# Kernel optimization log

Measured on AMD Instinct MI355X. Metric: run time of the kernel, lower is better.

The kernel has to match this reference:

```python
import jax, jax.numpy as jnp
import numpy as np

N_NODES = 50000
N_EDGES = 800000
D = 128
L = 3


def setup_inputs() -> dict:
    key = jax.random.key(0)
    ks = jax.random.split(key, 16)
    x = jax.random.normal(ks[0], (N_NODES, D), dtype=jnp.float32)
    edge_index = jax.random.randint(ks[1], (2, N_EDGES), 0, N_NODES, dtype=jnp.int32)
    # ensure every node has at least one incoming edge (degree > 0)
    edge_index = edge_index.at[1, :N_NODES].set(jnp.arange(N_NODES, dtype=jnp.int32))
    edge_attr = jax.random.normal(ks[2], (N_EDGES, 1), dtype=jnp.float32)
    s = 1.0 / np.sqrt(D)
    lin_w = jax.random.normal(ks[3], (L, 1, D), dtype=jnp.float32)          # edge_dim=1 -> D
    lin_b = jax.random.normal(ks[4], (L, D), dtype=jnp.float32) * s
    eps = jnp.zeros((L,), dtype=jnp.float32)                                 # initial_eps = 0, trainable
    w1 = jax.random.normal(ks[5], (L, D, D), dtype=jnp.float32) * s
    b1 = jax.random.normal(ks[6], (L, D), dtype=jnp.float32) * s
    w2 = jax.random.normal(ks[7], (L, D, D), dtype=jnp.float32) * s
    b2 = jax.random.normal(ks[8], (L, D), dtype=jnp.float32) * s
    d_cat = D + L * D
    final_w = jax.random.normal(ks[9], (d_cat, D), dtype=jnp.float32) / np.sqrt(d_cat)
    final_b = jax.random.normal(ks[10], (D,), dtype=jnp.float32) * s
    return {"x": x, "edge_index": edge_index, "edge_attr": edge_attr,
            "lin_w": lin_w, "lin_b": lin_b, "eps": eps,
            "w1": w1, "b1": b1, "w2": w2, "b2": b2,
            "final_w": final_w, "final_b": final_b}


def reference(x, edge_index, edge_attr, lin_w, lin_b, eps, w1, b1, w2, b2, final_w, final_b):
    src, tgt = edge_index[0], edge_index[1]
    n = x.shape[0]
    # degree of target nodes (float), shape [N, 1]
    deg = jax.ops.segment_sum(jnp.ones(src.shape[0], x.dtype), tgt, num_segments=n)[:, None]
    xs = [x]
    h = x
    for l in range(L):
        e = edge_attr @ lin_w[l] + lin_b[l]                  # [E, D] edge-feature projection
        msg = jax.nn.relu(h[src] + e)                        # gather + fuse + relu
        agg = jax.ops.segment_sum(msg, tgt, num_segments=n)  # scatter-add
        out = agg / deg + (1.0 + eps[l]) * h                 # degree-normalize + eps-residual
        h = jax.nn.relu(out @ w1[l] + b1[l]) @ w2[l] + b2[l] # 2-layer MLP (no BN, no dropout)
        xs.append(h)
    cat = jnp.concatenate(xs, axis=-1)                       # [N, D + L*D]
    return cat @ final_w + final_b
```

## Files before the change

kernel.cpp:

```cpp
#include <hip/hip_runtime.h>

#define NN 50000
#define NE 800000
#define DIM 128
#define NLAYERS 3

typedef __attribute__((ext_vector_type(8))) short bf16x8;
typedef __attribute__((ext_vector_type(4))) float f32x4;

__device__ __forceinline__ unsigned short f2bf_hi(float f) {
    unsigned int u = __float_as_uint(f);
    u += 0x7FFF + ((u >> 16) & 1);
    return (unsigned short)(u >> 16);
}
__device__ __forceinline__ float bf2f(unsigned short u) {
    return __uint_as_float(((unsigned int)u) << 16);
}

__global__ __launch_bounds__(256) void rank_kernel(const int* __restrict__ tgt,
                                                   int* __restrict__ counts,
                                                   int* __restrict__ rank, int E) {
    int base = (blockIdx.x * 256 + threadIdx.x) * 4;
    if (base >= E) return;
    int4 t = *(const int4*)(tgt + base);
    int4 r;
    r.x = atomicAdd(&counts[t.x], 1);
    r.y = atomicAdd(&counts[t.y], 1);
    r.z = atomicAdd(&counts[t.z], 1);
    r.w = atomicAdd(&counts[t.w], 1);
    *(int4*)(rank + base) = r;
}

__global__ __launch_bounds__(256) void scan_partial_kernel(const int* __restrict__ counts,
                                                           int* __restrict__ psum, int n) {
    __shared__ int ws[4];
    int b = blockIdx.x, t = threadIdx.x;
    int idx = b * 1024 + t * 4;
    int v = 0;
    if (idx < n) {
        int4 c = *(const int4*)(counts + idx);
        v = c.x + c.y + c.z + c.w;
    }
#pragma unroll
    for (int o = 32; o > 0; o >>= 1) v += __shfl_xor(v, o);
    int lane = t & 63, wid = t >> 6;
    if (lane == 0) ws[wid] = v;
    __syncthreads();
    if (t == 0) psum[b] = ws[0] + ws[1] + ws[2] + ws[3];
}

__global__ __launch_bounds__(64) void scan_small_kernel(const int* __restrict__ psum,
                                                        int* __restrict__ pbase,
                                                        int* __restrict__ offsets,
                                                        int nb, int n) {
    int lane = threadIdx.x;
    int v = (lane < nb) ? psum[lane] : 0;
    int incl = v;
#pragma unroll
    for (int o = 1; o < 64; o <<= 1) {
        int t = __shfl_up(incl, o);
        if (lane >= o) incl += t;
    }
    if (lane < nb) pbase[lane] = incl - v;
    if (lane == 63) offsets[n] = incl;
}

__global__ __launch_bounds__(256) void scan_apply_kernel(const int* __restrict__ counts,
                                                         const int* __restrict__ pbase,
                                                         int* __restrict__ offsets, int n) {
    __shared__ int ws[4];
    int b = blockIdx.x, t = threadIdx.x;
    int lane = t & 63, wid = t >> 6;
    int idx = b * 1024 + t * 4;
    int4 c = make_int4(0, 0, 0, 0);
    if (idx < n) c = *(const int4*)(counts + idx);
    int tsum = c.x + c.y + c.z + c.w;
    int incl = tsum;
#pragma unroll
    for (int o = 1; o < 64; o <<= 1) {
        int tt = __shfl_up(incl, o);
        if (lane >= o) incl += tt;
    }
    if (lane == 63) ws[wid] = incl;
    __syncthreads();
    int wbase = pbase[b];
    for (int w = 0; w < wid; w++) wbase += ws[w];
    if (idx < n) {
        int e0 = wbase + incl - tsum;
        int4 o;
        o.x = e0;
        o.y = e0 + c.x;
        o.z = o.y + c.y;
        o.w = o.z + c.z;
        *(int4*)(offsets + idx) = o;
    }
}

__global__ __launch_bounds__(256) void scatter2_kernel(
    const int* __restrict__ src, const int* __restrict__ tgt,
    const float* __restrict__ ea, const int* __restrict__ rank,
    const int* __restrict__ offsets, int2* __restrict__ sedge, int E) {
    int base = (blockIdx.x * 256 + threadIdx.x) * 4;
    if (base >= E) return;
    int4 s = *(const int4*)(src + base);
    int4 t = *(const int4*)(tgt + base);
    int4 r = *(const int4*)(rank + base);
    float4 a = *(const float4*)(ea + base);
    sedge[offsets[t.x] + r.x] = make_int2(s.x << 8, __float_as_int(a.x));
    sedge[offsets[t.y] + r.y] = make_int2(s.y << 8, __float_as_int(a.y));
    sedge[offsets[t.z] + r.z] = make_int2(s.z << 8, __float_as_int(a.z));
    sedge[offsets[t.w] + r.w] = make_int2(s.w << 8, __float_as_int(a.w));
}

__global__ __launch_bounds__(256) void xcvt_kernel(const float* __restrict__ x,
                                                   unsigned short* __restrict__ xb, int n) {
    int i = (blockIdx.x * 256 + threadIdx.x) * 4;
    if (i >= n) return;
    float4 v = *(const float4*)(x + i);
    ushort4 o;
    o.x = f2bf_hi(v.x); o.y = f2bf_hi(v.y);
    o.z = f2bf_hi(v.z); o.w = f2bf_hi(v.w);
    *(ushort4*)(xb + i) = o;
}

__global__ __launch_bounds__(256) void agg_kernel(
    const unsigned short* __restrict__ hprev, const int* __restrict__ offs,
    const int2* __restrict__ sedge,
    const float* __restrict__ lw, const float* __restrict__ lb,
    const float* __restrict__ epsp, int layer,
    float* __restrict__ outb, int N) {
    int wv = threadIdx.x >> 6;
    int node = blockIdx.x * 4 + wv;
    if (node >= N) return;
    int lane = threadIdx.x & 63;
    int q = lane >> 4, r = lane & 15;
    int d0 = r * 8;
    float lwv[8], lbv[8];
    *(float4*)&lwv[0] = *(const float4*)(lw + d0);
    *(float4*)&lwv[4] = *(const float4*)(lw + d0 + 4);
    *(float4*)&lbv[0] = *(const float4*)(lb + d0);
    *(float4*)&lbv[4] = *(const float4*)(lb + d0 + 4);
    int s0 = offs[node], s1 = offs[node + 1];
    int cnt = s1 - s0;
    float a[8];
#pragma unroll
    for (int c = 0; c < 8; c++) a[c] = 0.f;

    const char* hbase = (const char*)hprev + r * 16;

    int idx = s0 + q;
    int2 e0 = sedge[min(idx, s1 - 1)];
    int2 e1 = sedge[min(idx + 4, s1 - 1)];
    int2 e2 = sedge[min(idx + 8, s1 - 1)];
    uint4 h0 = *(const uint4*)(hbase + (unsigned)e0.x);
    uint4 h1 = *(const uint4*)(hbase + (unsigned)e1.x);

    for (int it = idx; it < s1; it += 4) {
        uint4 h2 = *(const uint4*)(hbase + (unsigned)e2.x);
        int2 e3 = sedge[min(it + 12, s1 - 1)];
        float wgt = __int_as_float(e0.y);
        unsigned uu[4] = {h0.x, h0.y, h0.z, h0.w};
#pragma unroll
        for (int c = 0; c < 4; c++) {
            float f0 = __uint_as_float(uu[c] << 16);
            float f1 = __uint_as_float(uu[c] & 0xffff0000u);
            a[2 * c]     += fmaxf(f0 + fmaf(wgt, lwv[2 * c], lbv[2 * c]), 0.f);
            a[2 * c + 1] += fmaxf(f1 + fmaf(wgt, lwv[2 * c + 1], lbv[2 * c + 1]), 0.f);
        }
        e0 = e1; e1 = e2; e2 = e3;
        h0 = h1; h1 = h2;
    }

#pragma unroll
    for (int c = 0; c < 8; c++) {
        a[c] += __shfl_xor(a[c], 16);
        a[c] += __shfl_xor(a[c], 32);
    }

    if (q == 0) {
        float inv = 1.f / (float)cnt;
        float ge = 1.f + epsp[layer];
        uint4 hs = *(const uint4*)(hbase + ((unsigned)node << 8));
        unsigned su[4] = {hs.x, hs.y, hs.z, hs.w};
        float o[8];
#pragma unroll
        for (int c = 0; c < 4; c++) {
            float f0 = __uint_as_float(su[c] << 16);
            float f1 = __uint_as_float(su[c] & 0xffff0000u);
            o[2 * c]     = a[2 * c] * inv + ge * f0;
            o[2 * c + 1] = a[2 * c + 1] * inv + ge * f1;
        }
        float* op = outb + (size_t)node * DIM + d0;
        *(float4*)op = *(float4*)&o[0];
        *(float4*)(op + 4) = *(float4*)&o[4];
    }
}

__global__ __launch_bounds__(256) void wprep_kernel(
    const float* __restrict__ w1, const float* __restrict__ w2, const float* __restrict__ fw,
    unsigned short* __restrict__ w1t_h, unsigned short* __restrict__ w1t_l,
    unsigned short* __restrict__ w2t_h, unsigned short* __restrict__ w2t_l,
    unsigned short* __restrict__ fwt_h, unsigned short* __restrict__ fwt_l) {
    int gid = blockIdx.x * 256 + threadIdx.x;
    float v; int oidx;
    unsigned short *oh, *ol;
    if (gid < 49152) {
        int l = gid >> 14, rem = gid & 16383, k = rem >> 7, c = rem & 127;
        v = w1[gid]; oidx = l * 16384 + c * 128 + k; oh = w1t_h; ol = w1t_l;
    } else if (gid < 98304) {
        int g = gid - 49152;
        int l = g >> 14, rem = g & 16383, k = rem >> 7, c = rem & 127;
        v = w2[g]; oidx = l * 16384 + c * 128 + k; oh = w2t_h; ol = w2t_l;
    } else if (gid < 163840) {
        int g = gid - 98304;
        int k = g >> 7, c = g & 127;
        v = fw[g]; oidx = c * 512 + k; oh = fwt_h; ol = fwt_l;
    } else return;
    unsigned short h = f2bf_hi(v);
    float lo = v - bf2f(h);
    oh[oidx] = h;
    ol[oidx] = f2bf_hi(lo);
}

#define AST 40
#define WST 40

__global__ __launch_bounds__(256) void mlp_fused(
    const float* __restrict__ in,
    const unsigned short* __restrict__ w1h, const unsigned short* __restrict__ w1l,
    const float* __restrict__ b1,
    const unsigned short* __restrict__ w2h, const unsigned short* __restrict__ w2l,
    const float* __restrict__ b2,
    unsigned short* __restrict__ out, int N) {
    __shared__ float s_h[64][132];
    __shared__ unsigned short s_ah[64 * AST], s_al[64 * AST];
    __shared__ unsigned short s_wh[128 * WST], s_wl[128 * WST];
    int tid = threadIdx.x;
    int n0 = blockIdx.x * 64;
    int lane = tid & 63, w = tid >> 6;
    int q = lane >> 4, lr = lane & 15;
    int wr = w >> 1, wc = w & 1;
    int sar = tid >> 2, sak = (tid & 3) * 8;
    int swc = tid >> 1, sws = (tid & 1) * 16;

    f32x4 acc[2][4];
#pragma unroll
    for (int i = 0; i < 2; i++)
#pragma unroll
        for (int j = 0; j < 4; j++) acc[i][j] = (f32x4)(0.f);

    for (int k0 = 0; k0 < 128; k0 += 32) {
        float f[8] = {0.f, 0.f, 0.f, 0.f, 0.f, 0.f, 0.f, 0.f};
        if (n0 + sar < NN) {
            const float* ap = in + (size_t)(n0 + sar) * 128 + k0 + sak;
            float4 v0 = *(const float4*)ap;
            float4 v1 = *(const float4*)(ap + 4);
            f[0] = v0.x; f[1] = v0.y; f[2] = v0.z; f[3] = v0.w;
            f[4] = v1.x; f[5] = v1.y; f[6] = v1.z; f[7] = v1.w;
        }
        unsigned int uh[4], ul[4];
#pragma unroll
        for (int i = 0; i < 4; i++) {
            unsigned short h0 = f2bf_hi(f[2 * i]);
            unsigned short h1 = f2bf_hi(f[2 * i + 1]);
            unsigned short l0 = f2bf_hi(f[2 * i] - bf2f(h0));
            unsigned short l1 = f2bf_hi(f[2 * i + 1] - bf2f(h1));
            uh[i] = (unsigned int)h0 | ((unsigned int)h1 << 16);
            ul[i] = (unsigned int)l0 | ((unsigned int)l1 << 16);
        }
        *(uint4*)&s_ah[sar * AST + sak] = make_uint4(uh[0], uh[1], uh[2], uh[3]);
        *(uint4*)&s_al[sar * AST + sak] = make_uint4(ul[0], ul[1], ul[2], ul[3]);
        {
            const unsigned short* wph = w1h + (size_t)swc * 128 + k0 + sws;
            const unsigned short* wpl = w1l + (size_t)swc * 128 + k0 + sws;
            uint4 h0 = *(const uint4*)wph;
            uint4 h1 = *(const uint4*)(wph + 8);
            uint4 l0 = *(const uint4*)wpl;
            uint4 l1 = *(const uint4*)(wpl + 8);
            *(uint4*)&s_wh[swc * WST + sws] = h0;
            *(uint4*)&s_wh[swc * WST + sws + 8] = h1;
            *(uint4*)&s_wl[swc * WST + sws] = l0;
            *(uint4*)&s_wl[swc * WST + sws + 8] = l1;
        }
        __syncthreads();
        bf16x8 ah[2], al_[2], bh[4], bl[4];
#pragma unroll
        for (int i = 0; i < 2; i++) {
            int row = wr * 32 + i * 16 + lr;
            ah[i]  = *(const bf16x8*)&s_ah[row * AST + q * 8];
            al_[i] = *(const bf16x8*)&s_al[row * AST + q * 8];
        }
#pragma unroll
        for (int j = 0; j < 4; j++) {
            int col = wc * 64 + j * 16 + lr;
            bh[j] = *(const bf16x8*)&s_wh[col * WST + q * 8];
            bl[j] = *(const bf16x8*)&s_wl[col * WST + q * 8];
        }
#pragma unroll
        for (int i = 0; i < 2; i++)
#pragma unroll
            for (int j = 0; j < 4; j++) {
                acc[i][j] = __builtin_amdgcn_mfma_f32_16x16x32_bf16(ah[i], bh[j], acc[i][j], 0, 0, 0);
                acc[i][j] = __builtin_amdgcn_mfma_f32_16x16x32_bf16(ah[i], bl[j], acc[i][j], 0, 0, 0);
                acc[i][j] = __builtin_amdgcn_mfma_f32_16x16x32_bf16(al_[i], bh[j], acc[i][j], 0, 0, 0);
            }
        __syncthreads();
    }
#pragma unroll
    for (int i = 0; i < 2; i++) {
        int rbase = wr * 32 + i * 16 + q * 4;
#pragma unroll
        for (int j = 0; j < 4; j++) {
            int col = wc * 64 + j * 16 + lr;
            float bv = b1[col];
#pragma unroll
            for (int r = 0; r < 4; r++)
                s_h[rbase + r][col] = fmaxf(acc[i][j][r] + bv, 0.f);
        }
    }
    __syncthreads();

#pragma unroll
    for (int i = 0; i < 2; i++)
#pragma unroll
        for (int j = 0; j < 4; j++) acc[i][j] = (f32x4)(0.f);

    for (int k0 = 0; k0 < 128; k0 += 32) {
        float f[8];
        *(float4*)&f[0] = *(const float4*)&s_h[sar][k0 + sak];
        *(float4*)&f[4] = *(const float4*)&s_h[sar][k0 + sak + 4];
        unsigned int uh[4], ul[4];
#pragma unroll
        for (int i = 0; i < 4; i++) {
            unsigned short h0 = f2bf_hi(f[2 * i]);
            unsigned short h1 = f2bf_hi(f[2 * i + 1]);
            unsigned short l0 = f2bf_hi(f[2 * i] - bf2f(h0));
            unsigned short l1 = f2bf_hi(f[2 * i + 1] - bf2f(h1));
            uh[i] = (unsigned int)h0 | ((unsigned int)h1 << 16);
            ul[i] = (unsigned int)l0 | ((unsigned int)l1 << 16);
        }
        __syncthreads();
        *(uint4*)&s_ah[sar * AST + sak] = make_uint4(uh[0], uh[1], uh[2], uh[3]);
        *(uint4*)&s_al[sar * AST + sak] = make_uint4(ul[0], ul[1], ul[2], ul[3]);
        {
            const unsigned short* wph = w2h + (size_t)swc * 128 + k0 + sws;
            const unsigned short* wpl = w2l + (size_t)swc * 128 + k0 + sws;
            uint4 h0 = *(const uint4*)wph;
            uint4 h1 = *(const uint4*)(wph + 8);
            uint4 l0 = *(const uint4*)wpl;
            uint4 l1 = *(const uint4*)(wpl + 8);
            *(uint4*)&s_wh[swc * WST + sws] = h0;
            *(uint4*)&s_wh[swc * WST + sws + 8] = h1;
            *(uint4*)&s_wl[swc * WST + sws] = l0;
            *(uint4*)&s_wl[swc * WST + sws + 8] = l1;
        }
        __syncthreads();
        bf16x8 ah[2], al_[2], bh[4], bl[4];
#pragma unroll
        for (int i = 0; i < 2; i++) {
            int row = wr * 32 + i * 16 + lr;
            ah[i]  = *(const bf16x8*)&s_ah[row * AST + q * 8];
            al_[i] = *(const bf16x8*)&s_al[row * AST + q * 8];
        }
#pragma unroll
        for (int j = 0; j < 4; j++) {
            int col = wc * 64 + j * 16 + lr;
            bh[j] = *(const bf16x8*)&s_wh[col * WST + q * 8];
            bl[j] = *(const bf16x8*)&s_wl[col * WST + q * 8];
        }
#pragma unroll
        for (int i = 0; i < 2; i++)
#pragma unroll
            for (int j = 0; j < 4; j++) {
                acc[i][j] = __builtin_amdgcn_mfma_f32_16x16x32_bf16(ah[i], bh[j], acc[i][j], 0, 0, 0);
                acc[i][j] = __builtin_amdgcn_mfma_f32_16x16x32_bf16(ah[i], bl[j], acc[i][j], 0, 0, 0);
                acc[i][j] = __builtin_amdgcn_mfma_f32_16x16x32_bf16(al_[i], bh[j], acc[i][j], 0, 0, 0);
            }
    }

#pragma unroll
    for (int i = 0; i < 2; i++) {
        int rbase = wr * 32 + i * 16 + q * 4;
#pragma unroll
        for (int j = 0; j < 4; j++) {
            int col = wc * 64 + j * 16 + lr;
            float bv = b2[col];
#pragma unroll
            for (int r = 0; r < 4; r++) {
                int node = n0 + rbase + r;
                if (node < NN)
                    out[(size_t)node * 128 + col] = f2bf_hi(acc[i][j][r] + bv);
            }
        }
    }
}

__global__ __launch_bounds__(256) void final_mfma(
    const unsigned short* __restrict__ a0, const unsigned short* __restrict__ a1,
    const unsigned short* __restrict__ a2, const unsigned short* __restrict__ a3,
    const unsigned short* __restrict__ wt_h, const unsigned short* __restrict__ wt_l,
    const float* __restrict__ bias, float* __restrict__ out, int N) {
    __shared__ unsigned short s_ah[64 * AST];
    __shared__ unsigned short s_wh[128 * WST], s_wl[128 * WST];
    const unsigned short* srcs[4] = {a0, a1, a2, a3};
    const int K = 512;
    int tid = threadIdx.x;
    int n0 = blockIdx.x * 64;
    int lane = tid & 63, w = tid >> 6;
    int q = lane >> 4, lr = lane & 15;
    int wr = w >> 1, wc = w & 1;

    f32x4 acc[2][4];
#pragma unroll
    for (int i = 0; i < 2; i++)
#pragma unroll
        for (int j = 0; j < 4; j++) acc[i][j] = (f32x4)(0.f);

    int sar = tid >> 2;
    int sak = (tid & 3) * 8;
    int swc = tid >> 1;
    int sws = (tid & 1) * 16;

    for (int k0 = 0; k0 < K; k0 += 32) {
        const unsigned short* asrc = srcs[k0 >> 7];
        int kl = k0 & 127;
        uint4 av = make_uint4(0, 0, 0, 0);
        if (n0 + sar < N)
            av = *(const uint4*)(asrc + (size_t)(n0 + sar) * 128 + kl + sak);
        *(uint4*)&s_ah[sar * AST + sak] = av;
        {
            const unsigned short* wph = wt_h + (size_t)swc * K + k0 + sws;
            const unsigned short* wpl = wt_l + (size_t)swc * K + k0 + sws;
            uint4 h0 = *(const uint4*)wph;
            uint4 h1 = *(const uint4*)(wph + 8);
            uint4 l0 = *(const uint4*)wpl;
            uint4 l1 = *(const uint4*)(wpl + 8);
            *(uint4*)&s_wh[swc * WST + sws] = h0;
            *(uint4*)&s_wh[swc * WST + sws + 8] = h1;
            *(uint4*)&s_wl[swc * WST + sws] = l0;
            *(uint4*)&s_wl[swc * WST + sws + 8] = l1;
        }
        __syncthreads();
        bf16x8 ah[2], bh[4], bl[4];
#pragma unroll
        for (int i = 0; i < 2; i++) {
            int row = wr * 32 + i * 16 + lr;
            ah[i] = *(const bf16x8*)&s_ah[row * AST + q * 8];
        }
#pragma unroll
        for (int j = 0; j < 4; j++) {
            int col = wc * 64 + j * 16 + lr;
            bh[j] = *(const bf16x8*)&s_wh[col * WST + q * 8];
            bl[j] = *(const bf16x8*)&s_wl[col * WST + q * 8];
        }
#pragma unroll
        for (int i = 0; i < 2; i++)
#pragma unroll
            for (int j = 0; j < 4; j++) {
                acc[i][j] = __builtin_amdgcn_mfma_f32_16x16x32_bf16(ah[i], bh[j], acc[i][j], 0, 0, 0);
                acc[i][j] = __builtin_amdgcn_mfma_f32_16x16x32_bf16(ah[i], bl[j], acc[i][j], 0, 0, 0);
            }
        __syncthreads();
    }

#pragma unroll
    for (int i = 0; i < 2; i++) {
        int rbase = wr * 32 + i * 16 + q * 4;
#pragma unroll
        for (int j = 0; j < 4; j++) {
            int col = wc * 64 + j * 16 + lr;
            float bv = bias[col];
#pragma unroll
            for (int r = 0; r < 4; r++) {
                int node = n0 + rbase + r;
                if (node < N)
                    out[(size_t)node * 128 + col] = acc[i][j][r] + bv;
            }
        }
    }
}

extern "C" void kernel_launch(void* const* d_in, const int* in_sizes, int n_in,
                              void* d_out, int out_size, void* d_ws, size_t ws_size,
                              hipStream_t stream) {
    const float* x   = (const float*)d_in[0];
    const int* edge_index = (const int*)d_in[1];
    const float* ea  = (const float*)d_in[2];
    const float* lw  = (const float*)d_in[3];
    const float* lb  = (const float*)d_in[4];
    const float* eps = (const float*)d_in[5];
    const float* w1  = (const float*)d_in[6];
    const float* b1  = (const float*)d_in[7];
    const float* w2  = (const float*)d_in[8];
    const float* b2  = (const float*)d_in[9];
    const float* fw  = (const float*)d_in[10];
    const float* fb  = (const float*)d_in[11];
    float* out = (float*)d_out;

    const int N = NN, E = NE;
    const int* src = edge_index;
    const int* tgt = edge_index + E;
    const int NB = (N + 1023) / 1024;

    char* ws = (char*)d_ws;
    size_t off = 0;
    auto alloc = [&](size_t bytes) {
        void* p = ws + off;
        off += (bytes + 255) & ~(size_t)255;
        return p;
    };
    int*   counts  = (int*)alloc((size_t)N * 4);
    int*   offsets = (int*)alloc((size_t)(N + 1) * 4);
    int*   rank    = (int*)alloc((size_t)E * 4);
    int*   psum    = (int*)alloc((size_t)NB * 4);
    int*   pbase   = (int*)alloc((size_t)NB * 4);
    int2*  sedge   = (int2*)alloc((size_t)E * 8);
    unsigned short* w1t_h = (unsigned short*)alloc(49152 * 2);
    unsigned short* w1t_l = (unsigned short*)alloc(49152 * 2);
    unsigned short* w2t_h = (unsigned short*)alloc(49152 * 2);
    unsigned short* w2t_l = (unsigned short*)alloc(49152 * 2);
    unsigned short* fwt_h = (unsigned short*)alloc(65536 * 2);
    unsigned short* fwt_l = (unsigned short*)alloc(65536 * 2);
    unsigned short* xb    = (unsigned short*)alloc((size_t)N * DIM * 2);
    unsigned short* hbuf[3];
    for (int i = 0; i < 3; i++) hbuf[i] = (unsigned short*)alloc((size_t)N * DIM * 2);
    float* outb = (float*)alloc((size_t)N * DIM * 4);
    (void)ws_size; (void)in_sizes; (void)n_in; (void)out_size;

    hipMemsetAsync(counts, 0, (size_t)N * 4, stream);
    rank_kernel<<<(E / 4 + 255) / 256, 256, 0, stream>>>(tgt, counts, rank, E);
    wprep_kernel<<<640, 256, 0, stream>>>(w1, w2, fw, w1t_h, w1t_l, w2t_h, w2t_l, fwt_h, fwt_l);
    xcvt_kernel<<<(N * DIM / 4 + 255) / 256, 256, 0, stream>>>(x, xb, N * DIM);
    scan_partial_kernel<<<NB, 256, 0, stream>>>(counts, psum, N);
    scan_small_kernel<<<1, 64, 0, stream>>>(psum, pbase, offsets, NB, N);
    scan_apply_kernel<<<NB, 256, 0, stream>>>(counts, pbase, offsets, N);
    scatter2_kernel<<<(E / 4 + 255) / 256, 256, 0, stream>>>(src, tgt, ea, rank, offsets, sedge, E);

    const int GB = (N + 63) / 64;
    for (int l = 0; l < NLAYERS; l++) {
        const unsigned short* hin = (l == 0) ? xb : hbuf[l - 1];
        agg_kernel<<<(N + 3) / 4, 256, 0, stream>>>(hin, offsets, sedge,
            lw + l * DIM, lb + l * DIM, eps, l, outb, N);
        mlp_fused<<<GB, 256, 0, stream>>>(
            outb,
            w1t_h + l * 16384, w1t_l + l * 16384, b1 + l * DIM,
            w2t_h + l * 16384, w2t_l + l * 16384, b2 + l * DIM,
            hbuf[l], N);
    }
    final_mfma<<<GB, 256, 0, stream>>>(
        xb, hbuf[0], hbuf[1], hbuf[2], fwt_h, fwt_l, fb, out, N);
}
```

Measured before the change: 378.5 us.

## Pre-split aggregation output to bf16 hi/lo and load MFMA weights directly from packed layout

The aggregation kernel now writes bf16 hi/lo pairs instead of fp32, so the MLP no longer splits its input in registers. Weights are pre-packed into MFMA fragment order, so each wave loads its A fragments straight from global memory rather than staging them through shared memory with barriers. The MLP and final GEMM use a transposed tiling (weights as A, nodes as B) and store hidden activations to LDS as bf16 hi/lo. The trade is more global weight loads per wave, relying on cache hits, in exchange for fewer LDS round trips and syncs.

New measurement: 371.4 us. About the same (-1.9%).

```diff
diff --git a/kernel.cpp b/kernel.cpp
--- a/kernel.cpp
+++ b/kernel.cpp
@@ -128,7 +128,7 @@
     const int2* __restrict__ sedge,
     const float* __restrict__ lw, const float* __restrict__ lb,
     const float* __restrict__ epsp, int layer,
-    float* __restrict__ outb, int N) {
+    unsigned short* __restrict__ aggh, unsigned short* __restrict__ aggl, int N) {
     int wv = threadIdx.x >> 6;
     int node = blockIdx.x * 4 + wv;
     if (node >= N) return;
@@ -182,18 +182,29 @@
         float ge = 1.f + epsp[layer];
         uint4 hs = *(const uint4*)(hbase + ((unsigned)node << 8));
         unsigned su[4] = {hs.x, hs.y, hs.z, hs.w};
-        float o[8];
+        unsigned short hh[8], hl[8];
 #pragma unroll
         for (int c = 0; c < 4; c++) {
             float f0 = __uint_as_float(su[c] << 16);
             float f1 = __uint_as_float(su[c] & 0xffff0000u);
-            o[2 * c]     = a[2 * c] * inv + ge * f0;
-            o[2 * c + 1] = a[2 * c + 1] * inv + ge * f1;
-        }
-        float* op = outb + (size_t)node * DIM + d0;
-        *(float4*)op = *(float4*)&o[0];
-        *(float4*)(op + 4) = *(float4*)&o[4];
-    }
+            float v0 = a[2 * c] * inv + ge * f0;
+            float v1 = a[2 * c + 1] * inv + ge * f1;
+            unsigned short h0v = f2bf_hi(v0), h1v = f2bf_hi(v1);
+            hh[2 * c] = h0v; hh[2 * c + 1] = h1v;
+            hl[2 * c] = f2bf_hi(v0 - bf2f(h0v));
+            hl[2 * c + 1] = f2bf_hi(v1 - bf2f(h1v));
+        }
+        unsigned short* ph = aggh + (size_t)node * DIM + d0;
+        unsigned short* pl = aggl + (size_t)node * DIM + d0;
+        *(ushort4*)ph       = *(const ushort4*)&hh[0];
+        *(ushort4*)(ph + 4) = *(const ushort4*)&hh[4];
+        *(ushort4*)pl       = *(const ushort4*)&hl[0];
+        *(ushort4*)(pl + 4) = *(const ushort4*)&hl[4];
+    }
+}
+
+__device__ __forceinline__ int packidx(int k, int c) {
+    return (((k >> 5) << 3) + (c >> 4)) * 512 + (((k >> 3) & 3) << 7) + ((c & 15) << 3) + (k & 7);
 }
 
 __global__ __launch_bounds__(256) void wprep_kernel(
@@ -206,15 +217,15 @@
     unsigned short *oh, *ol;
     if (gid < 49152) {
         int l = gid >> 14, rem = gid & 16383, k = rem >> 7, c = rem & 127;
-        v = w1[gid]; oidx = l * 16384 + c * 128 + k; oh = w1t_h; ol = w1t_l;
+        v = w1[gid]; oidx = l * 16384 + packidx(k, c); oh = w1t_h; ol = w1t_l;
     } else if (gid < 98304) {
         int g = gid - 49152;
         int l = g >> 14, rem = g & 16383, k = rem >> 7, c = rem & 127;
-        v = w2[g]; oidx = l * 16384 + c * 128 + k; oh = w2t_h; ol = w2t_l;
+        v = w2[g]; oidx = l * 16384 + packidx(k, c); oh = w2t_h; ol = w2t_l;
     } else if (gid < 163840) {
         int g = gid - 98304;
         int k = g >> 7, c = g & 127;
-        v = fw[g]; oidx = c * 512 + k; oh = fwt_h; ol = fwt_l;
+        v = fw[g]; oidx = packidx(k, c); oh = fwt_h; ol = fwt_l;
     } else return;
     unsigned short h = f2bf_hi(v);
     float lo = v - bf2f(h);
@@ -222,259 +233,179 @@
     ol[oidx] = f2bf_hi(lo);
 }
 
-#define AST 40
-#define WST 40
-
-__global__ __launch_bounds__(256) void mlp_fused(
-    const float* __restrict__ in,
+#define HSTR 136
+
+__global__ __launch_bounds__(256, 4) void mlp_fused(
+    const unsigned short* __restrict__ ah_g, const unsigned short* __restrict__ al_g,
     const unsigned short* __restrict__ w1h, const unsigned short* __restrict__ w1l,
     const float* __restrict__ b1,
     const unsigned short* __restrict__ w2h, const unsigned short* __restrict__ w2l,
     const float* __restrict__ b2,
     unsigned short* __restrict__ out, int N) {
-    __shared__ float s_h[64][132];
-    __shared__ unsigned short s_ah[64 * AST], s_al[64 * AST];
-    __shared__ unsigned short s_wh[128 * WST], s_wl[128 * WST];
+    __shared__ unsigned short s_hh[64 * HSTR], s_hl[64 * HSTR];
     int tid = threadIdx.x;
-    int n0 = blockIdx.x * 64;
     int lane = tid & 63, w = tid >> 6;
     int q = lane >> 4, lr = lane & 15;
     int wr = w >> 1, wc = w & 1;
-    int sar = tid >> 2, sak = (tid & 3) * 8;
-    int swc = tid >> 1, sws = (tid & 1) * 16;
-
-    f32x4 acc[2][4];
-#pragma unroll
-    for (int i = 0; i < 2; i++)
-#pragma unroll
-        for (int j = 0; j < 4; j++) acc[i][j] = (f32x4)(0.f);
-
+    int n0 = blockIdx.x * 64;
+    int nb0 = n0 + wc * 32 + lr;
+
+    f32x4 acc[4][2];
+#pragma unroll
+    for (int i = 0; i < 4; i++)
+#pragma unroll
+        for (int j = 0; j < 2; j++) acc[i][j] = (f32x4)(0.f);
+
+#pragma unroll
     for (int k0 = 0; k0 < 128; k0 += 32) {
-        float f[8] = {0.f, 0.f, 0.f, 0.f, 0.f, 0.f, 0.f, 0.f};
-        if (n0 + sar < NN) {
-            const float* ap = in + (size_t)(n0 + sar) * 128 + k0 + sak;
-            float4 v0 = *(const float4*)ap;
-            float4 v1 = *(const float4*)(ap + 4);
-            f[0] = v0.x; f[1] = v0.y; f[2] = v0.z; f[3] = v0.w;
-            f[4] = v1.x; f[5] = v1.y; f[6] = v1.z; f[7] = v1.w;
-        }
-        unsigned int uh[4], ul[4];
+        bf16x8 Bh[2], Bl[2];
+#pragma unroll
+        for (int j = 0; j < 2; j++) {
+            size_t ro = (size_t)min(nb0 + j * 16, N - 1) * DIM + k0 + q * 8;
+            Bh[j] = *(const bf16x8*)(ah_g + ro);
+            Bl[j] = *(const bf16x8*)(al_g + ro);
+        }
 #pragma unroll
         for (int i = 0; i < 4; i++) {
-            unsigned short h0 = f2bf_hi(f[2 * i]);
-            unsigned short h1 = f2bf_hi(f[2 * i + 1]);
-            unsigned short l0 = f2bf_hi(f[2 * i] - bf2f(h0));
-            unsigned short l1 = f2bf_hi(f[2 * i + 1] - bf2f(h1));
-            uh[i] = (unsigned int)h0 | ((unsigned int)h1 << 16);
-            ul[i] = (unsigned int)l0 | ((unsigned int)l1 << 16);
-        }
-        *(uint4*)&s_ah[sar * AST + sak] = make_uint4(uh[0], uh[1], uh[2], uh[3]);
-        *(uint4*)&s_al[sar * AST + sak] = make_uint4(ul[0], ul[1], ul[2], ul[3]);
-        {
-            const unsigned short* wph = w1h + (size_t)swc * 128 + k0 + sws;
-            const unsigned short* wpl = w1l + (size_t)swc * 128 + k0 + sws;
-            uint4 h0 = *(const uint4*)wph;
-            uint4 h1 = *(const uint4*)(wph + 8);
-            uint4 l0 = *(const uint4*)wpl;
-            uint4 l1 = *(const uint4*)(wpl + 8);
-            *(uint4*)&s_wh[swc * WST + sws] = h0;
-            *(uint4*)&s_wh[swc * WST + sws + 8] = h1;
-            *(uint4*)&s_wl[swc * WST + sws] = l0;
-            *(uint4*)&s_wl[swc * WST + sws + 8] = l1;
-        }
-        __syncthreads();
-        bf16x8 ah[2], al_[2], bh[4], bl[4];
-#pragma unroll
-        for (int i = 0; i < 2; i++) {
-            int row = wr * 32 + i * 16 + lr;
-            ah[i]  = *(const bf16x8*)&s_ah[row * AST + q * 8];
-            al_[i] = *(const bf16x8*)&s_al[row * AST + q * 8];
-        }
-#pragma unroll
-        for (int j = 0; j < 4; j++) {
-            int col = wc * 64 + j * 16 + lr;
-            bh[j] = *(const bf16x8*)&s_wh[col * WST + q * 8];
-            bl[j] = *(const bf16x8*)&s_wl[col * WST + q * 8];
-        }
-#pragma unroll
-        for (int i = 0; i < 2; i++)
-#pragma unroll
-            for (int j = 0; j < 4; j++) {
-                acc[i][j] = __builtin_amdgcn_mfma_f32_16x16x32_bf16(ah[i], bh[j], acc[i][j], 0, 0, 0);
-                acc[i][j] = __builtin_amdgcn_mfma_f32_16x16x32_bf16(ah[i], bl[j], acc[i][j], 0, 0, 0);
-                acc[i][j] = __builtin_amdgcn_mfma_f32_16x16x32_bf16(al_[i], bh[j], acc[i][j], 0, 0, 0);
-            }
-        __syncthreads();
-    }
-#pragma unroll
-    for (int i = 0; i < 2; i++) {
-        int rbase = wr * 32 + i * 16 + q * 4;
-#pragma unroll
-        for (int j = 0; j < 4; j++) {
-            int col = wc * 64 + j * 16 + lr;
-            float bv = b1[col];
-#pragma unroll
-            for (int r = 0; r < 4; r++)
-                s_h[rbase + r][col] = fmaxf(acc[i][j][r] + bv, 0.f);
+            size_t co = ((size_t)((k0 >> 5) * 8 + wr * 4 + i) << 9) + lane * 8;
+            bf16x8 Ah = *(const bf16x8*)(w1h + co);
+            bf16x8 Al = *(const bf16x8*)(w1l + co);
+#pragma unroll
+            for (int j = 0; j < 2; j++) {
+                acc[i][j] = __builtin_amdgcn_mfma_f32_16x16x32_bf16(Ah, Bh[j], acc[i][j], 0, 0, 0);
+                acc[i][j] = __builtin_amdgcn_mfma_f32_16x16x32_bf16(Ah, Bl[j], acc[i][j], 0, 0, 0);
+                acc[i][j] = __builtin_amdgcn_mfma_f32_16x16x32_bf16(Al, Bh[j], acc[i][j], 0, 0, 0);
+            }
+        }
+    }
+
+#pragma unroll
+    for (int i = 0; i < 4; i++) {
+        int hc0 = wr * 64 + i * 16 + q * 4;
+        float4 bv = *(const float4*)(b1 + hc0);
+        float bvr[4] = {bv.x, bv.y, bv.z, bv.w};
+#pragma unroll
+        for (int j = 0; j < 2; j++) {
+            int nl = wc * 32 + j * 16 + lr;
+            unsigned short hh[4], hl[4];
+#pragma unroll
+            for (int r = 0; r < 4; r++) {
+                float v = fmaxf(acc[i][j][r] + bvr[r], 0.f);
+                unsigned short h = f2bf_hi(v);
+                hh[r] = h;
+                hl[r] = f2bf_hi(v - bf2f(h));
+            }
+            *(ushort4*)&s_hh[nl * HSTR + hc0] = *(const ushort4*)&hh[0];
+            *(ushort4*)&s_hl[nl * HSTR + hc0] = *(const ushort4*)&hl[0];
         }
     }
     __syncthreads();
 
 #pragma unroll
-    for (int i = 0; i < 2; i++)
-#pragma unroll
-        for (int j = 0; j < 4; j++) acc[i][j] = (f32x4)(0.f);
-
+    for (int i = 0; i < 4; i++)
+#pragma unroll
+        for (int j = 0; j < 2; j++) acc[i][j] = (f32x4)(0.f);
+
+#pragma unroll
     for (int k0 = 0; k0 < 128; k0 += 32) {
-        float f[8];
-        *(float4*)&f[0] = *(const float4*)&s_h[sar][k0 + sak];
-        *(float4*)&f[4] = *(const float4*)&s_h[sar][k0 + sak + 4];
-        unsigned int uh[4], ul[4];
+        bf16x8 Bh[2], Bl[2];
+#pragma unroll
+        for (int j = 0; j < 2; j++) {
+            int so = (wc * 32 + j * 16 + lr) * HSTR + k0 + q * 8;
+            Bh[j] = *(const bf16x8*)&s_hh[so];
+            Bl[j] = *(const bf16x8*)&s_hl[so];
+        }
 #pragma unroll
         for (int i = 0; i < 4; i++) {
-            unsigned short h0 = f2bf_hi(f[2 * i]);
-            unsigned short h1 = f2bf_hi(f[2 * i + 1]);
-            unsigned short l0 = f2bf_hi(f[2 * i] - bf2f(h0));
-            unsigned short l1 = f2bf_hi(f[2 * i + 1] - bf2f(h1));
-            uh[i] = (unsigned int)h0 | ((unsigned int)h1 << 16);
-            ul[i] = (unsigned int)l0 | ((unsigned int)l1 << 16);
-        }
-        __syncthreads();
-        *(uint4*)&s_ah[sar * AST + sak] = make_uint4(uh[0], uh[1], uh[2], uh[3]);
-        *(uint4*)&s_al[sar * AST + sak] = make_uint4(ul[0], ul[1], ul[2], ul[3]);
-        {
-            const unsigned short* wph = w2h + (size_t)swc * 128 + k0 + sws;
-            const unsigned short* wpl = w2l + (size_t)swc * 128 + k0 + sws;
-            uint4 h0 = *(const uint4*)wph;
-            uint4 h1 = *(const uint4*)(wph + 8);
-            uint4 l0 = *(const uint4*)wpl;
-            uint4 l1 = *(const uint4*)(wpl + 8);
-            *(uint4*)&s_wh[swc * WST + sws] = h0;
-            *(uint4*)&s_wh[swc * WST + sws + 8] = h1;
-            *(uint4*)&s_wl[swc * WST + sws] = l0;
-            *(uint4*)&s_wl[swc * WST + sws + 8] = l1;
-        }
-        __syncthreads();
-        bf16x8 ah[2], al_[2], bh[4], bl[4];
-#pragma unroll
-        for (int i = 0; i < 2; i++) {
-            int row = wr * 32 + i * 16 + lr;
-            ah[i]  = *(const bf16x8*)&s_ah[row * AST + q * 8];
-            al_[i] = *(const bf16x8*)&s_al[row * AST + q * 8];
-        }
-#pragma unroll
-        for (int j = 0; j < 4; j++) {
-            int col = wc * 64 + j * 16 + lr;
-            bh[j] = *(const bf16x8*)&s_wh[col * WST + q * 8];
-            bl[j] = *(const bf16x8*)&s_wl[col * WST + q * 8];
-        }
-#pragma unroll
-        for (int i = 0; i < 2; i++)
-#pragma unroll
-            for (int j = 0; j < 4; j++) {
-                acc[i][j] = __builtin_amdgcn_mfma_f32_16x16x32_bf16(ah[i], bh[j], acc[i][j], 0, 0, 0);
-                acc[i][j] = __builtin_amdgcn_mfma_f32_16x16x32_bf16(ah[i], bl[j], acc[i][j], 0, 0, 0);
-                acc[i][j] = __builtin_amdgcn_mfma_f32_16x16x32_bf16(al_[i], bh[j], acc[i][j], 0, 0, 0);
-            }
-    }
-
-#pragma unroll
-    for (int i = 0; i < 2; i++) {
-        int rbase = wr * 32 + i * 16 + q * 4;
-#pragma unroll
-        for (int j = 0; j < 4; j++) {
-            int col = wc * 64 + j * 16 + lr;
-            float bv = b2[col];
-#pragma unroll
-            for (int r = 0; r < 4; r++) {
-                int node = n0 + rbase + r;
-                if (node < NN)
-                    out[(size_t)node * 128 + col] = f2bf_hi(acc[i][j][r] + bv);
-            }
-        }
-    }
-}
-
-__global__ __launch_bounds__(256) void final_mfma(
+            size_t co = ((size_t)((k0 >> 5) * 8 + wr * 4 + i) << 9) + lane * 8;
+            bf16x8 Ah = *(const bf16x8*)(w2h + co);
+            bf16x8 Al = *(const bf16x8*)(w2l + co);
+#pragma unroll
+            for (int j = 0; j < 2; j++) {
+                acc[i][j] = __builtin_amdgcn_mfma_f32_16x16x32_bf16(Ah, Bh[j], acc[i][j], 0, 0, 0);
+                acc[i][j] = __builtin_amdgcn_mfma_f32_16x16x32_bf16(Ah, Bl[j], acc[i][j], 0, 0, 0);
+                acc[i][j] = __builtin_amdgcn_mfma_f32_16x16x32_bf16(Al, Bh[j], acc[i][j], 0, 0, 0);
+            }
+        }
+    }
+
+#pragma unroll
+    for (int i = 0; i < 4; i++) {
+        int hc0 = wr * 64 + i * 16 + q * 4;
+        float4 bv = *(const float4*)(b2 + hc0);
+        float bvr[4] = {bv.x, bv.y, bv.z, bv.w};
+#pragma unroll
+        for (int j = 0; j < 2; j++) {
+            int node = nb0 + j * 16;
+            if (node < N) {
+                unsigned short o[4];
+#pragma unroll
+                for (int r = 0; r < 4; r++) o[r] = f2bf_hi(acc[i][j][r] + bvr[r]);
+                *(ushort4*)&out[(size_t)node * DIM + hc0] = *(const ushort4*)&o[0];
+            }
+        }
+    }
+}
+
+__global__ __launch_bounds__(256, 4) void final_mfma(
     const unsigned short* __restrict__ a0, const unsigned short* __restrict__ a1,
     const unsigned short* __restrict__ a2, const unsigned short* __restrict__ a3,
-    const unsigned short* __restrict__ wt_h, const unsigned short* __restrict__ wt_l,
+    const unsigned short* __restrict__ wh, const unsigned short* __restrict__ wl,
     const float* __restrict__ bias, float* __restrict__ out, int N) {
-    __shared__ unsigned short s_ah[64 * AST];
-    __shared__ unsigned short s_wh[128 * WST], s_wl[128 * WST];
-    const unsigned short* srcs[4] = {a0, a1, a2, a3};
-    const int K = 512;
     int tid = threadIdx.x;
-    int n0 = blockIdx.x * 64;
     int lane = tid & 63, w = tid >> 6;
     int q = lane >> 4, lr = lane & 15;
     int wr = w >> 1, wc = w & 1;
-
-    f32x4 acc[2][4];
-#pragma unroll
-    for (int i = 0; i < 2; i++)
-#pragma unroll
-        for (int j = 0; j < 4; j++) acc[i][j] = (f32x4)(0.f);
-
-    int sar = tid >> 2;
-    int sak = (tid & 3) * 8;
-    int swc = tid >> 1;
-    int sws = (tid & 1) * 16;
-
-    for (int k0 = 0; k0 < K; k0 += 32) {
-        const unsigned short* asrc = srcs[k0 >> 7];
-        int kl = k0 & 127;
-        uint4 av = make_uint4(0, 0, 0, 0);
-        if (n0 + sar < N)
-            av = *(const uint4*)(asrc + (size_t)(n0 + sar) * 128 + kl + sak);
-        *(uint4*)&s_ah[sar * AST + sak] = av;
-        {
-            const unsigned short* wph = wt_h + (size_t)swc * K + k0 + sws;
-            const unsigned short* wpl = wt_l + (size_t)swc * K + k0 + sws;
-            uint4 h0 = *(const uint4*)wph;
-            uint4 h1 = *(const uint4*)(wph + 8);
-            uint4 l0 = *(const uint4*)wpl;
-            uint4 l1 = *(const uint4*)(wpl + 8);
-            *(uint4*)&s_wh[swc * WST + sws] = h0;
-            *(uint4*)&s_wh[swc * WST + sws + 8] = h1;
-            *(uint4*)&s_wl[swc * WST + sws] = l0;
-            *(uint4*)&s_wl[swc * WST + sws + 8] = l1;
-        }
-        __syncthreads();
-        bf16x8 ah[2], bh[4], bl[4];
-#pragma unroll
-        for (int i = 0; i < 2; i++) {
-            int row = wr * 32 + i * 16 + lr;
-            ah[i] = *(const bf16x8*)&s_ah[row * AST + q * 8];
-        }
-#pragma unroll
-        for (int j = 0; j < 4; j++) {
-            int col = wc * 64 + j * 16 + lr;
-            bh[j] = *(const bf16x8*)&s_wh[col * WST + q * 8];
-            bl[j] = *(const bf16x8*)&s_wl[col * WST + q * 8];
-        }
-#pragma unroll
-        for (int i = 0; i < 2; i++)
-#pragma unroll
-            for (int j = 0; j < 4; j++) {
-                acc[i][j] = __builtin_amdgcn_mfma_f32_16x16x32_bf16(ah[i], bh[j], acc[i][j], 0, 0, 0);
-                acc[i][j] = __builtin_amdgcn_mfma_f32_16x16x32_bf16(ah[i], bl[j], acc[i][j], 0, 0, 0);
-            }
-        __syncthreads();
-    }
-
-#pragma unroll
-    for (int i = 0; i < 2; i++) {
-        int rbase = wr * 32 + i * 16 + q * 4;
-#pragma unroll
-        for (int j = 0; j < 4; j++) {
-            int col = wc * 64 + j * 16 + lr;
-            float bv = bias[col];
-#pragma unroll
-            for (int r = 0; r < 4; r++) {
-                int node = n0 + rbase + r;
-                if (node < N)
-                    out[(size_t)node * 128 + col] = acc[i][j][r] + bv;
+    int n0 = blockIdx.x * 64;
+    int nb0 = n0 + wc * 32 + lr;
+
+    f32x4 acc[4][2];
+#pragma unroll
+    for (int i = 0; i < 4; i++)
+#pragma unroll
+        for (int j = 0; j < 2; j++) acc[i][j] = (f32x4)(0.f);
+
+#pragma unroll
+    for (int s = 0; s < 4; s++) {
+        const unsigned short* asrc = (s == 0) ? a0 : (s == 1) ? a1 : (s == 2) ? a2 : a3;
+#pragma unroll
+        for (int kk = 0; kk < 128; kk += 32) {
+            int k0 = s * 128 + kk;
+            bf16x8 B[2];
+#pragma unroll
+            for (int j = 0; j < 2; j++) {
+                size_t ro = (size_t)min(nb0 + j * 16, N - 1) * DIM + kk + q * 8;
+                B[j] = *(const bf16x8*)(asrc + ro);
+            }
+#pragma unroll
+            for (int i = 0; i < 4; i++) {
+                size_t co = ((size_t)((k0 >> 5) * 8 + wr * 4 + i) << 9) + lane * 8;
+                bf16x8 Ah = *(const bf16x8*)(wh + co);
+                bf16x8 Al = *(const bf16x8*)(wl + co);
+#pragma unroll
+                for (int j = 0; j < 2; j++) {
+                    acc[i][j] = __builtin_amdgcn_mfma_f32_16x16x32_bf16(Ah, B[j], acc[i][j], 0, 0, 0);
+                    acc[i][j] = __builtin_amdgcn_mfma_f32_16x16x32_bf16(Al, B[j], acc[i][j], 0, 0, 0);
+                }
+            }
+        }
+    }
+
+#pragma unroll
+    for (int i = 0; i < 4; i++) {
+        int hc0 = wr * 64 + i * 16 + q * 4;
+        float4 bv = *(const float4*)(bias + hc0);
+        float bvr[4] = {bv.x, bv.y, bv.z, bv.w};
+#pragma unroll
+        for (int j = 0; j < 2; j++) {
+            int node = nb0 + j * 16;
+            if (node < N) {
+                float4 o;
+                o.x = acc[i][j][0] + bvr[0];
+                o.y = acc[i][j][1] + bvr[1];
+                o.z = acc[i][j][2] + bvr[2];
+                o.w = acc[i][j][3] + bvr[3];
+                *(float4*)&out[(size_t)node * DIM + hc0] = o;
             }
         }
     }
@@ -524,7 +455,8 @@
     unsigned short* xb    = (unsigned short*)alloc((size_t)N * DIM * 2);
     unsigned short* hbuf[3];
     for (int i = 0; i < 3; i++) hbuf[i] = (unsigned short*)alloc((size_t)N * DIM * 2);
-    float* outb = (float*)alloc((size_t)N * DIM * 4);
+    unsigned short* aggh = (unsigned short*)alloc((size_t)N * DIM * 2);
+    unsigned short* aggl = (unsigned short*)alloc((size_t)N * DIM * 2);
     (void)ws_size; (void)in_sizes; (void)n_in; (void)out_size;
 
     hipMemsetAsync(counts, 0, (size_t)N * 4, stream);
@@ -540,9 +472,9 @@
     for (int l = 0; l < NLAYERS; l++) {
         const unsigned short* hin = (l == 0) ? xb : hbuf[l - 1];
         agg_kernel<<<(N + 3) / 4, 256, 0, stream>>>(hin, offsets, sedge,
-            lw + l * DIM, lb + l * DIM, eps, l, outb, N);
+            lw + l * DIM, lb + l * DIM, eps, l, aggh, aggl, N);
         mlp_fused<<<GB, 256, 0, stream>>>(
-            outb,
+            aggh, aggl,
             w1t_h + l * 16384, w1t_l + l * 16384, b1 + l * DIM,
             w2t_h + l * 16384, w2t_l + l * 16384, b2 + l * DIM,
             hbuf[l], N);
```
